# Optimization experiments

Measured on AMD Instinct MI355X. Metric: run time of the kernel, lower is better.

Reference implementation:

```python
import jax, jax.numpy as jnp
import numpy as np

FL = 9       # filterlen
STRIDE = 1
B, CIN, COUT, T = 2, 16, 16, 2048


def hmul(p, q):
    """Hamilton product of quaternions stored in the last axis (..., 4).
    Equivalent to q2m(p, Qmt).matmul(q) in the torch code."""
    pw, px, py, pz = p[..., 0], p[..., 1], p[..., 2], p[..., 3]
    qw, qx, qy, qz = q[..., 0], q[..., 1], q[..., 2], q[..., 3]
    return jnp.stack([
        pw * qw - px * qx - py * qy - pz * qz,
        pw * qx + px * qw + py * qz - pz * qy,
        pw * qy - px * qz + py * qw + pz * qx,
        pw * qz + px * qy - py * qx + pz * qw,
    ], axis=-1)


def setup_inputs() -> dict:
    key = jax.random.key(0)
    k1, k2, k3, k4 = jax.random.split(key, 4)
    he = np.float32(np.sqrt(2.0 / FL / CIN))
    pdims = (1, COUT, CIN, 1, FL, 1)  # broadcast over quaternion axis
    x = jax.random.normal(k1, (B, CIN, T, 4, 1), dtype=jnp.float32)
    a = jax.random.normal(k2, pdims, dtype=jnp.float32) * he
    b = jax.random.normal(k3, pdims, dtype=jnp.float32) * np.float32(0.5)
    c = jax.random.normal(k4, pdims, dtype=jnp.float32) * np.float32(np.sqrt(1.378 ** 2 - 0.25))
    return {"x": x, "a": a, "b": b, "c": c}


def reference(x, a, b, c):
    # x: (B, Cin, T, 4, 1) -> drop trailing singleton, quaternion on last axis
    xq = x[..., 0]  # (B, Cin, T, 4)
    fl, s = FL, STRIDE
    T_in = xq.shape[2]
    T_out = (T_in - fl) // s + 1

    # unfold: sliding windows of length fl along time -> (B, Cin, T_out, fl, 4)
    idx = jnp.arange(T_out)[:, None] * s + jnp.arange(fl)[None, :]
    q = xq[:, :, idx]                      # (B, Cin, T_out, fl, 4)
    q = q[:, None]                         # (B, 1, Cin, T_out, fl, 4)

    # center element of each window -> (B, 1, Cin, T_out, 1, 4)
    qp = xq[:, :, fl // 2: fl // 2 + (T_out - 1) * s + 1: s]
    qp = qp[:, None, :, :, None, :]

    eye = jnp.array([1.0, 0.0, 0.0, 0.0], dtype=x.dtype)
    conj_sign = jnp.array([1.0, -1.0, -1.0, -1.0], dtype=x.dtype)

    # qpc: (B, Cout, Cin, T_out, fl, 4) -- c adds to the real part only
    qpc = qp + c * eye

    # res = qpc * (q * conj(qpc)) / |qpc|^2   (quaternion conjugation/rotation)
    inner = hmul(q, qpc * conj_sign)
    nsq = jnp.sum(qpc * qpc, axis=-1, keepdims=True)
    res = hmul(qpc, inner) / nsq

    # res = q * res + b * res ; scale by a
    res = hmul(q, res) + b * res
    res = res * a

    # sum over filterlen (axis 4) and in-channels (axis 2)
    out = res.sum(axis=(2, 4))             # (B, Cout, T_out, 4)
    return out[..., None]                  # (B, Cout, T_out, 4, 1)
```

## Files before the change

### kernel.cpp

```cpp
#include <hip/hip_runtime.h>

#define FL 9
#define CIN 16
#define COUT 16
#define T_IN 2048
#define T_OUT 2040
#define NB 2
#define TTILE 16
#define XW (TTILE + FL - 1)

__global__ __launch_bounds__(1024) void qconv_kernel(
    const float* __restrict__ x, const float* __restrict__ pa,
    const float* __restrict__ pb, const float* __restrict__ pc,
    float* __restrict__ out)
{
    __shared__ float4 xs[CIN][XW];
    __shared__ float4 pabc[COUT * CIN * FL];
    __shared__ float4 red[3][COUT * TTILE];

    const int tid   = threadIdx.x;
    const int batch = blockIdx.x >> 7;
    const int tile  = blockIdx.x & 127;
    const int t0    = tile * TTILE;

    for (int i = tid; i < COUT * CIN * FL; i += 1024) {
        pabc[i] = make_float4(pa[i], pb[i], pc[i], 0.0f);
    }
    {
        const float4* xg = (const float4*)x;
        int i = tid;
        if (i < CIN * XW) {
            int cin = i / XW;
            int ii  = i - cin * XW;
            int t   = t0 + ii;
            if (t > T_IN - 1) t = T_IN - 1;
            xs[cin][ii] = xg[(batch * CIN + cin) * T_IN + t];
        }
    }
    __syncthreads();

    const int tl = tid & 15;
    const int co = (tid >> 4) & 15;
    const int cg = tid >> 8;

    float accw = 0.f, accx = 0.f, accy = 0.f, accz = 0.f;

    #pragma unroll
    for (int ci = 0; ci < 4; ++ci) {
        const int cin = cg * 4 + ci;
        const float4 qp = xs[cin][tl + 4];
        const float px = qp.y, py = qp.z, pz = qp.w;
        const float h  = px * px + py * py + pz * pz;

        #pragma unroll
        for (int j = 0; j < FL; ++j) {
            const float4 qj = xs[cin][tl + j];
            const float4 p  = pabc[(co * CIN + cin) * FL + j];
            const float av = p.x, bv = p.y, cv = p.z;

            const float aw = qj.x, ax = qj.y, ay = qj.z, az = qj.w;
            const float pw = qp.x + cv;

            const float nsq = __builtin_fmaf(pw, pw, h);
            float rn = __builtin_amdgcn_rcpf(nsq);
            rn = rn * (2.0f - nsq * rn);

            const float iw =  aw*pw + ax*px + ay*py + az*pz;
            const float ix = -aw*px + ax*pw - ay*pz + az*py;
            const float iy = -aw*py + ax*pz + ay*pw - az*px;
            const float iz = -aw*pz - ax*py + ay*px + az*pw;

            const float tw = aw * nsq;
            const float tx = pw*ix + px*iw + py*iz - pz*iy;
            const float ty = pw*iy - px*iz + py*iw + pz*ix;
            const float tz = pw*iz + px*iy - py*ix + pz*iw;

            const float rw = aw*tw - ax*tx - ay*ty - az*tz + bv*tw;
            const float rx = aw*tx + ax*tw + ay*tz - az*ty + bv*tx;
            const float ry = aw*ty - ax*tz + ay*tw + az*tx + bv*ty;
            const float rz = aw*tz + ax*ty - ay*tx + az*tw + bv*tz;

            const float s = av * rn;
            accw = __builtin_fmaf(rw, s, accw);
            accx = __builtin_fmaf(rx, s, accx);
            accy = __builtin_fmaf(ry, s, accy);
            accz = __builtin_fmaf(rz, s, accz);
        }
    }

    if (cg != 0) {
        red[cg - 1][co * TTILE + tl] = make_float4(accw, accx, accy, accz);
    }
    __syncthreads();
    if (cg == 0) {
        const int t = t0 + tl;
        if (t < T_OUT) {
            const float4 r1 = red[0][tid];
            const float4 r2 = red[1][tid];
            const float4 r3 = red[2][tid];
            float4 o;
            o.x = accw + r1.x + r2.x + r3.x;
            o.y = accx + r1.y + r2.y + r3.y;
            o.z = accy + r1.z + r2.z + r3.z;
            o.w = accz + r1.w + r2.w + r3.w;
            ((float4*)out)[(batch * COUT + co) * T_OUT + t] = o;
        }
    }
}

extern "C" void kernel_launch(void* const* d_in, const int* in_sizes, int n_in,
                              void* d_out, int out_size, void* d_ws, size_t ws_size,
                              hipStream_t stream) {
    const float* x  = (const float*)d_in[0];
    const float* pa = (const float*)d_in[1];
    const float* pb = (const float*)d_in[2];
    const float* pc = (const float*)d_in[3];
    float* out = (float*)d_out;

    dim3 grid(NB * ((T_OUT + TTILE - 1) / TTILE));
    dim3 block(1024);
    qconv_kernel<<<grid, block, 0, stream>>>(x, pa, pb, pc, out);
}
```

Baseline: 80.21 us.

## Factor quaternion rotation into pw-polynomial and split Cin across blocks with reduce pass

Rewrites the quaternion-conv kernel. It expands the rotation as a quadratic polynomial in the shifted real part pw, so the terms that depend only on the input are computed once per filter tap and reused across 8 output channels. Parameters are read with wave-uniform (readfirstlane) indices instead of being staged in shared memory. Input channels are split across 4 block groups that write partial sums to a workspace, and a second kernel sums them, which adds a launch and extra global traffic.

```diff
diff --git a/kernel.cpp b/kernel.cpp
--- a/kernel.cpp
+++ b/kernel.cpp
@@ -5,106 +5,166 @@
 #define COUT 16
 #define T_IN 2048
 #define T_OUT 2040
-#define NB 2
-#define TTILE 16
+#define TTILE 64
 #define XW (TTILE + FL - 1)
 
-__global__ __launch_bounds__(1024) void qconv_kernel(
+__global__ __launch_bounds__(256) void qconv_main(
     const float* __restrict__ x, const float* __restrict__ pa,
     const float* __restrict__ pb, const float* __restrict__ pc,
-    float* __restrict__ out)
+    float4* __restrict__ part)
 {
-    __shared__ float4 xs[CIN][XW];
-    __shared__ float4 pabc[COUT * CIN * FL];
-    __shared__ float4 red[3][COUT * TTILE];
+    __shared__ float4 xs[4][XW];
+    __shared__ float4 red[3][8][TTILE];
 
-    const int tid   = threadIdx.x;
-    const int batch = blockIdx.x >> 7;
-    const int tile  = blockIdx.x & 127;
-    const int t0    = tile * TTILE;
+    const int bid    = blockIdx.x;
+    const int cohalf = bid & 1;
+    const int cinq   = (bid >> 1) & 3;
+    const int tile   = (bid >> 3) & 31;
+    const int b      = bid >> 8;
+    const int t0     = tile * TTILE;
 
-    for (int i = tid; i < COUT * CIN * FL; i += 1024) {
-        pabc[i] = make_float4(pa[i], pb[i], pc[i], 0.0f);
-    }
+    const int tid = threadIdx.x;
+    const int tl  = tid & 63;
+    const int cl  = tid >> 6;
+    const int cin = cinq * 4 + cl;
+
     {
-        const float4* xg = (const float4*)x;
-        int i = tid;
-        if (i < CIN * XW) {
-            int cin = i / XW;
-            int ii  = i - cin * XW;
-            int t   = t0 + ii;
+        const float4* xg = (const float4*)x + (b * CIN + cin) * T_IN;
+        for (int i = tl; i < XW; i += 64) {
+            int t = t0 + i;
             if (t > T_IN - 1) t = T_IN - 1;
-            xs[cin][ii] = xg[(batch * CIN + cin) * T_IN + t];
+            xs[cl][i] = xg[t];
         }
     }
     __syncthreads();
 
-    const int tl = tid & 15;
-    const int co = (tid >> 4) & 15;
-    const int cg = tid >> 8;
+    const float4 qp  = xs[cl][tl + 4];
+    const float  qpw = qp.x;
+    const float  vx = qp.y, vy = qp.z, vz = qp.w;
+    const float  h  = vx * vx + vy * vy + vz * vz;
 
-    float accw = 0.f, accx = 0.f, accy = 0.f, accz = 0.f;
+    const int cin_s = __builtin_amdgcn_readfirstlane(cin);
+    const int cob   = cohalf * 8;
+
+    float4 acc[8];
+    #pragma unroll
+    for (int co = 0; co < 8; ++co) acc[co] = make_float4(0.f, 0.f, 0.f, 0.f);
 
     #pragma unroll
-    for (int ci = 0; ci < 4; ++ci) {
-        const int cin = cg * 4 + ci;
-        const float4 qp = xs[cin][tl + 4];
-        const float px = qp.y, py = qp.z, pz = qp.w;
-        const float h  = px * px + py * py + pz * pz;
+    for (int j = 0; j < FL; ++j) {
+        const float4 Q = xs[cl][tl + j];
+        const float qw = Q.x, ux = Q.y, uy = Q.z, uz = Q.w;
+
+        const float cx = vy * uz - vz * uy;
+        const float cy = vz * ux - vx * uz;
+        const float cz = vx * uy - vy * ux;
+        const float d  = vx * ux + vy * uy + vz * uz;
+        const float uu = ux * ux + uy * uy + uz * uz;
+
+        const float a1x = cx + cx, a1y = cy + cy, a1z = cz + cz;
+        const float d2  = d + d;
+        const float a0w = qw * h;
+        const float a0x = d2 * vx - h * ux;
+        const float a0y = d2 * vy - h * uy;
+        const float a0z = d2 * vz - h * uz;
+
+        const float b2w = qw * qw - uu;
+        const float q2  = qw + qw;
+        const float b2x = q2 * ux, b2y = q2 * uy, b2z = q2 * uz;
+
+        const float b1w = -(ux * a1x + uy * a1y + uz * a1z);
+        const float e1x = uy * a1z - uz * a1y;
+        const float e1y = uz * a1x - ux * a1z;
+        const float e1z = ux * a1y - uy * a1x;
+        const float b1x = qw * a1x + e1x;
+        const float b1y = qw * a1y + e1y;
+        const float b1z = qw * a1z + e1z;
+
+        const float b0w = qw * a0w - (ux * a0x + uy * a0y + uz * a0z);
+        const float e0x = uy * a0z - uz * a0y;
+        const float e0y = uz * a0x - ux * a0z;
+        const float e0z = ux * a0y - uy * a0x;
+        const float b0x = qw * a0x + a0w * ux + e0x;
+        const float b0y = qw * a0y + a0w * uy + e0y;
+        const float b0z = qw * a0z + a0w * uz + e0z;
 
         #pragma unroll
-        for (int j = 0; j < FL; ++j) {
-            const float4 qj = xs[cin][tl + j];
-            const float4 p  = pabc[(co * CIN + cin) * FL + j];
-            const float av = p.x, bv = p.y, cv = p.z;
+        for (int co = 0; co < 8; ++co) {
+            const int pidx = ((cob + co) * CIN + cin_s) * FL + j;
+            const float av = pa[pidx], bv = pb[pidx], cv = pc[pidx];
 
-            const float aw = qj.x, ax = qj.y, ay = qj.z, az = qj.w;
-            const float pw = qp.x + cv;
-
-            const float nsq = __builtin_fmaf(pw, pw, h);
+            const float pw  = qpw + cv;
+            const float p2  = pw * pw;
+            const float nsq = p2 + h;
             float rn = __builtin_amdgcn_rcpf(nsq);
             rn = rn * (2.0f - nsq * rn);
+            const float s = av * rn;
 
-            const float iw =  aw*pw + ax*px + ay*py + az*pz;
-            const float ix = -aw*px + ax*pw - ay*pz + az*py;
-            const float iy = -aw*py + ax*pz + ay*pw - az*px;
-            const float iz = -aw*pz - ax*py + ay*px + az*pw;
+            const float f2w = __builtin_fmaf(bv, qw, b2w);
+            const float f2x = __builtin_fmaf(bv, ux, b2x);
+            const float f2y = __builtin_fmaf(bv, uy, b2y);
+            const float f2z = __builtin_fmaf(bv, uz, b2z);
+            const float f1x = __builtin_fmaf(bv, a1x, b1x);
+            const float f1y = __builtin_fmaf(bv, a1y, b1y);
+            const float f1z = __builtin_fmaf(bv, a1z, b1z);
+            const float f0w = __builtin_fmaf(bv, a0w, b0w);
+            const float f0x = __builtin_fmaf(bv, a0x, b0x);
+            const float f0y = __builtin_fmaf(bv, a0y, b0y);
+            const float f0z = __builtin_fmaf(bv, a0z, b0z);
 
-            const float tw = aw * nsq;
-            const float tx = pw*ix + px*iw + py*iz - pz*iy;
-            const float ty = pw*iy - px*iz + py*iw + pz*ix;
-            const float tz = pw*iz + px*iy - py*ix + pz*iw;
+            const float rw = __builtin_fmaf(f2w, p2, __builtin_fmaf(b1w, pw, f0w));
+            const float rx = __builtin_fmaf(f2x, p2, __builtin_fmaf(f1x, pw, f0x));
+            const float ry = __builtin_fmaf(f2y, p2, __builtin_fmaf(f1y, pw, f0y));
+            const float rz = __builtin_fmaf(f2z, p2, __builtin_fmaf(f1z, pw, f0z));
 
-            const float rw = aw*tw - ax*tx - ay*ty - az*tz + bv*tw;
-            const float rx = aw*tx + ax*tw + ay*tz - az*ty + bv*tx;
-            const float ry = aw*ty - ax*tz + ay*tw + az*tx + bv*ty;
-            const float rz = aw*tz + ax*ty - ay*tx + az*tw + bv*tz;
-
-            const float s = av * rn;
-            accw = __builtin_fmaf(rw, s, accw);
-            accx = __builtin_fmaf(rx, s, accx);
-            accy = __builtin_fmaf(ry, s, accy);
-            accz = __builtin_fmaf(rz, s, accz);
+            acc[co].x = __builtin_fmaf(rw, s, acc[co].x);
+            acc[co].y = __builtin_fmaf(rx, s, acc[co].y);
+            acc[co].z = __builtin_fmaf(ry, s, acc[co].z);
+            acc[co].w = __builtin_fmaf(rz, s, acc[co].w);
         }
     }
 
-    if (cg != 0) {
-        red[cg - 1][co * TTILE + tl] = make_float4(accw, accx, accy, accz);
+    if (cl != 0) {
+        #pragma unroll
+        for (int co = 0; co < 8; ++co) red[cl - 1][co][tl] = acc[co];
     }
     __syncthreads();
-    if (cg == 0) {
+    if (cl == 0) {
         const int t = t0 + tl;
         if (t < T_OUT) {
-            const float4 r1 = red[0][tid];
-            const float4 r2 = red[1][tid];
-            const float4 r3 = red[2][tid];
-            float4 o;
-            o.x = accw + r1.x + r2.x + r3.x;
-            o.y = accx + r1.y + r2.y + r3.y;
-            o.z = accy + r1.z + r2.z + r3.z;
-            o.w = accz + r1.w + r2.w + r3.w;
-            ((float4*)out)[(batch * COUT + co) * T_OUT + t] = o;
+            #pragma unroll
+            for (int co = 0; co < 8; ++co) {
+                const float4 r0 = red[0][co][tl];
+                const float4 r1 = red[1][co][tl];
+                const float4 r2 = red[2][co][tl];
+                float4 o;
+                o.x = acc[co].x + r0.x + r1.x + r2.x;
+                o.y = acc[co].y + r0.y + r1.y + r2.y;
+                o.z = acc[co].z + r0.z + r1.z + r2.z;
+                o.w = acc[co].w + r0.w + r1.w + r2.w;
+                part[(cinq * 32 + b * 16 + cob + co) * 2048 + t] = o;
+            }
         }
+    }
+}
+
+__global__ __launch_bounds__(256) void qconv_reduce(
+    const float4* __restrict__ part, float4* __restrict__ out)
+{
+    const int N = 2 * COUT * T_OUT;
+    for (int i = blockIdx.x * 256 + threadIdx.x; i < N; i += gridDim.x * 256) {
+        const int t  = i % T_OUT;
+        const int bc = i / T_OUT;
+        const float4 p0 = part[(0 * 32 + bc) * 2048 + t];
+        const float4 p1 = part[(1 * 32 + bc) * 2048 + t];
+        const float4 p2 = part[(2 * 32 + bc) * 2048 + t];
+        const float4 p3 = part[(3 * 32 + bc) * 2048 + t];
+        float4 o;
+        o.x = (p0.x + p1.x) + (p2.x + p3.x);
+        o.y = (p0.y + p1.y) + (p2.y + p3.y);
+        o.z = (p0.z + p1.z) + (p2.z + p3.z);
+        o.w = (p0.w + p1.w) + (p2.w + p3.w);
+        out[i] = o;
     }
 }
 
@@ -115,9 +175,9 @@
     const float* pa = (const float*)d_in[1];
     const float* pb = (const float*)d_in[2];
     const float* pc = (const float*)d_in[3];
-    float* out = (float*)d_out;
+    float4* part = (float4*)d_ws;
+    float4* out  = (float4*)d_out;
 
-    dim3 grid(NB * ((T_OUT + TTILE - 1) / TTILE));
-    dim3 block(1024);
-    qconv_kernel<<<grid, block, 0, stream>>>(x, pa, pb, pc, out);
+    qconv_main<<<dim3(512), dim3(256), 0, stream>>>(x, pa, pb, pc, part);
+    qconv_reduce<<<dim3(256), dim3(256), 0, stream>>>(part, out);
 }
```

Result: faster. 76.05 us (-5.2%).
